# Kernel optimization log

Measured on AMD Instinct MI355X. Metric: run time of the kernel, lower is better.

Reference implementation:

```python
import jax, jax.numpy as jnp
import numpy as np

D_MODEL = 1024
N_LAYER = 8
VOCAB = 32000
D_INNER = 2048
D_STATE = 16
DT_RANK = 64  # ceil(d_model/16)
KCONV = 4
SEQ = 2048


def causal_depthwise_conv(u, w):
    # u: [l, d_inner], w: [d_inner, 1, K]; causal padding (K-1, 0), groups=d_inner
    x = u.T[None]  # [1, d_inner, l]
    y = jax.lax.conv_general_dilated(
        x, w, window_strides=(1,), padding=[(KCONV - 1, 0)],
        dimension_numbers=("NCH", "OIH", "NCH"), feature_group_count=u.shape[1])
    return y[0].T  # [l, d_inner]


def selective_scan(u, dt, A, B, C, Dp):
    # u,dt: [l,d_in]; A: [d_in,n]; B,C: [l,n]; D: [d_in]; bilinear discretization
    dt_A = dt[:, :, None] * A[None, :, :]          # [l, d_in, n]
    dt_B = dt[:, :, None] * B[:, None, :]          # [l, d_in, n]
    denom = 1.0 - dt_A / 2
    dA = (1.0 + dt_A / 2) / denom
    dB = dt_B / denom

    def step(h, inp):
        ui, dAi, dBi, Ci = inp
        h = dAi * h + dBi * ui[:, None]            # [d_in, n]
        return h, h @ Ci                           # y_i: [d_in]

    h0 = jnp.zeros((u.shape[1], A.shape[1]), dtype=u.dtype)
    _, y = jax.lax.scan(step, h0, (u, dA, dB, C))
    return y + u * Dp


def mamba_layer(x, Wres, Win, Wconv, WB, WC, Wdt1, Wdt2, bdt, logA, Dp, Wout):
    # RMS pre-norm (no learned scale)
    xn = x * jax.lax.rsqrt(jnp.mean(x * x, axis=-1, keepdims=True) + 1e-6)
    res = xn @ Wres.T                              # [l, d_inner]
    u = xn @ Win.T                                 # [l, d_inner]
    u = causal_depthwise_conv(u, Wconv)
    u = jax.nn.silu(u)
    A = -jnp.exp(logA)                             # [d_inner, n]
    B = u @ WB.T                                   # [l, n]
    C = u @ WC.T                                   # [l, n]
    dt = jax.nn.softplus((u @ Wdt1.T) @ Wdt2.T + bdt)
    y = selective_scan(u, dt, A, B, C, Dp)
    y = y * jax.nn.silu(res)
    return x + y @ Wout.T                          # residual


def setup_inputs() -> dict:
    key = jax.random.key(0)
    ks = jax.random.split(key, 12)
    L = N_LAYER
    token_ids = jax.random.randint(ks[0], (SEQ,), 0, VOCAB)
    embed = jax.random.normal(ks[1], (VOCAB, D_MODEL), jnp.float32) * 0.02
    Wres = jax.random.normal(ks[2], (L, D_INNER, D_MODEL), jnp.float32) * 0.02
    Win = jax.random.normal(ks[3], (L, D_INNER, D_MODEL), jnp.float32) * 0.02
    Wconv = jax.random.normal(ks[4], (L, D_INNER, 1, KCONV), jnp.float32) * 0.3
    WB = jax.random.normal(ks[5], (L, D_STATE, D_INNER), jnp.float32) * 0.02
    WC = jax.random.normal(ks[6], (L, D_STATE, D_INNER), jnp.float32) * 0.02
    Wdt1 = jax.random.normal(ks[7], (L, DT_RANK, D_INNER), jnp.float32) / np.sqrt(D_INNER)
    Wdt2 = jax.random.uniform(ks[8], (L, D_INNER, DT_RANK), jnp.float32,
                              minval=-1 / np.sqrt(DT_RANK), maxval=1 / np.sqrt(DT_RANK))
    # inverse-softplus of dt ~ U[1e-3, 1e-1] in log space
    dt0 = jnp.exp(jax.random.uniform(ks[9], (L, D_INNER)) * (np.log(0.1) - np.log(0.001)) + np.log(0.001))
    bdt = dt0 + jnp.log(-jnp.expm1(-dt0))
    logA = jnp.log(jnp.broadcast_to(jnp.arange(1, D_STATE + 1, dtype=jnp.float32),
                                    (L, D_INNER, D_STATE)))
    Dp = jnp.ones((L, D_INNER), jnp.float32)
    Wout = jax.random.normal(ks[10], (L, D_MODEL, D_INNER), jnp.float32) * 0.02
    return dict(token_ids=token_ids, embed=embed, Wres=Wres, Win=Win, Wconv=Wconv,
                WB=WB, WC=WC, Wdt1=Wdt1, Wdt2=Wdt2, bdt=bdt, logA=logA, Dp=Dp, Wout=Wout)


def reference(token_ids, embed, Wres, Win, Wconv, WB, WC, Wdt1, Wdt2, bdt, logA, Dp, Wout):
    x = embed[token_ids]  # [l, d_model]
    for i in range(Wres.shape[0]):
        x = mamba_layer(x, Wres[i], Win[i], Wconv[i], WB[i], WC[i],
                        Wdt1[i], Wdt2[i], bdt[i], logA[i], Dp[i], Wout[i])
    return x @ embed.T  # [l, vocab] logits (tied embedding)
```

## Files before the change

### kernel.cpp

```cpp
#include <hip/hip_runtime.h>

#define SEQ 2048
#define DMODEL 1024
#define DINNER 2048
#define DSTATE 16
#define DTRANK 64
#define NLAYER 8
#define VOCAB 32000
#define NCHUNK 32
#define CLEN 64
#define PZ 16

typedef float f32x4 __attribute__((ext_vector_type(4)));
typedef short bf16x8 __attribute__((ext_vector_type(8)));

__device__ __forceinline__ ushort f2bf(float f) {
  union { float f; unsigned u; } v; v.f = f;
  unsigned r = v.u + 0x7fffu + ((v.u >> 16) & 1u);
  return (ushort)(r >> 16);
}
__device__ __forceinline__ float bf2f(ushort b) {
  union { unsigned u; float f; } v; v.u = ((unsigned)b) << 16;
  return v.f;
}

__device__ __forceinline__ void lds_load16(const void* g, void* l) {
  __builtin_amdgcn_global_load_lds(
      (const __attribute__((address_space(1))) void*)g,
      (__attribute__((address_space(3))) void*)l, 16, 0, 0);
}

template<int BM, bool NTS>
__global__ __launch_bounds__(512, 2) void gemm8p_bt_bf16(
    const ushort* __restrict__ A, const ushort* __restrict__ B,
    float* __restrict__ C, int N, int K)
{
  constexpr int MFR = BM / 32;
  constexpr int MPP = MFR / 4;
  constexpr int ALOADS = BM / 128;
  __shared__ __align__(16) ushort As[2 * BM * 64];
  __shared__ __align__(16) ushort Bs[2 * 256 * 64];
  const int tid = threadIdx.x;
  const int lane = tid & 63;
  const int wid = tid >> 6;
  const int wr = wid >> 2, wc = wid & 3;
  const int rr = lane & 15, kq = lane >> 4;

  unsigned nwg = gridDim.x * gridDim.y;
  unsigned lb = blockIdx.y * gridDim.x + blockIdx.x;
  if ((nwg & 7u) == 0u) { unsigned cpx = nwg >> 3; lb = (lb & 7u) * cpx + (lb >> 3); }
  const int bm = (int)(lb % gridDim.x) * BM;
  const int bn = (int)(lb / gridDim.x) * 256;

  const ushort* Abase = A + (size_t)bm * K;
  const ushort* Bbase = B + (size_t)bn * K;

  auto stageA = [&](int buf, int h, int kt) {
    constexpr int HR = BM / 2;
#pragma unroll
    for (int L = 0; L < ALOADS; ++L) {
      int f = L * 512 + tid;
      int rl = f >> 3, g = f & 7;
      int gg = g ^ (rl & 7);
      lds_load16(Abase + (size_t)(h * HR + rl) * K + kt * 64 + gg * 8,
                 (void*)(As + buf * (BM * 64) + (h * HR + rl) * 64 + g * 8));
    }
  };
  auto stageB = [&](int buf, int h, int kt) {
#pragma unroll
    for (int L = 0; L < 2; ++L) {
      int f = L * 512 + tid;
      int rl = f >> 3, g = f & 7;
      int gg = g ^ (rl & 7);
      lds_load16(Bbase + (size_t)(h * 128 + rl) * K + kt * 64 + gg * 8,
                 (void*)(Bs + buf * (256 * 64) + (h * 128 + rl) * 64 + g * 8));
    }
  };
  auto rdA = [&](int buf, int r, int kbyte) {
    int sw = kbyte ^ ((r & 7) << 4);
    return *(const bf16x8*)(As + buf * (BM * 64) + r * 64 + (sw >> 1));
  };
  auto rdB = [&](int buf, int r, int kbyte) {
    int sw = kbyte ^ ((r & 7) << 4);
    return *(const bf16x8*)(Bs + buf * (256 * 64) + r * 64 + (sw >> 1));
  };

  f32x4 acc[MFR][4];
#pragma unroll
  for (int m = 0; m < MFR; ++m)
#pragma unroll
    for (int n = 0; n < 4; ++n) acc[m][n] = (f32x4){0.f, 0.f, 0.f, 0.f};

  const int NT = K >> 6;
  stageA(0, 0, 0); stageA(0, 1, 0); stageB(0, 0, 0); stageB(0, 1, 0);

  for (int t = 0; t < NT; ++t) {
    const int cur = t & 1;
    const bool more = (t + 1 < NT);
    if (more) stageA(cur ^ 1, 0, t + 1);
    if (more) {
      if constexpr (BM == 256) asm volatile("s_waitcnt vmcnt(2)" ::: "memory");
      else                     asm volatile("s_waitcnt vmcnt(1)" ::: "memory");
    } else {
      asm volatile("s_waitcnt vmcnt(0)" ::: "memory");
    }
    __syncthreads();

    bf16x8 bfr[4][2];
#pragma unroll
    for (int n = 0; n < 4; ++n)
#pragma unroll
      for (int kk = 0; kk < 2; ++kk)
        bfr[n][kk] = rdB(cur, wc * 64 + n * 16 + rr, kk * 64 + kq * 16);

#pragma unroll
    for (int mq = 0; mq < 4; ++mq) {
      if (mq == 1 && more) stageA(cur ^ 1, 1, t + 1);
      if (mq == 2 && more) stageB(cur ^ 1, 0, t + 1);
      if (mq == 3 && more) stageB(cur ^ 1, 1, t + 1);
      bf16x8 af[MPP][2];
#pragma unroll
      for (int mf = 0; mf < MPP; ++mf)
#pragma unroll
        for (int kk = 0; kk < 2; ++kk)
          af[mf][kk] = rdA(cur, wr * (BM / 2) + (mq * MPP + mf) * 16 + rr, kk * 64 + kq * 16);
      __builtin_amdgcn_s_setprio(1);
#pragma unroll
      for (int kk = 0; kk < 2; ++kk)
#pragma unroll
        for (int mf = 0; mf < MPP; ++mf)
#pragma unroll
          for (int n = 0; n < 4; ++n)
            acc[mq * MPP + mf][n] = __builtin_amdgcn_mfma_f32_16x16x32_bf16(
                af[mf][kk], bfr[n][kk], acc[mq * MPP + mf][n], 0, 0, 0);
      __builtin_amdgcn_s_setprio(0);
    }
    __syncthreads();
  }

  float* ep = (float*)Bs + wid * (16 * 68);
  const int cg = bn + wc * 64;
#pragma unroll
  for (int m = 0; m < MFR; ++m) {
    const int r0g = bm + wr * (BM / 2) + m * 16;
#pragma unroll
    for (int n = 0; n < 4; ++n)
#pragma unroll
      for (int j = 0; j < 4; ++j)
        ep[(kq * 4 + j) * 68 + n * 16 + rr] = acc[m][n][j];
#pragma unroll
    for (int i = 0; i < 4; ++i) {
      int row = i * 4 + kq;
      f32x4 v = *(const f32x4*)&ep[row * 68 + rr * 4];
      f32x4* dst = (f32x4*)&C[(size_t)(r0g + row) * N + cg + rr * 4];
      if constexpr (NTS) __builtin_nontemporal_store(v, dst);
      else *dst = v;
    }
  }
}

template<bool OUTBF>
__global__ __launch_bounds__(256, 2) void gemm2p_bt_bf16(
    const ushort* __restrict__ A, const ushort* __restrict__ B,
    void* __restrict__ Cv, int N, int K)
{
  __shared__ __align__(16) ushort As[2 * 128 * 64];
  __shared__ __align__(16) ushort Bs[2 * 128 * 64];
  const int tid = threadIdx.x;
  const int lane = tid & 63;
  const int wave = tid >> 6;
  const int wr = wave >> 1, wc = wave & 1;
  const int rr = lane & 15, kq = lane >> 4;

  unsigned nwg = gridDim.x * gridDim.y;
  unsigned lb = blockIdx.y * gridDim.x + blockIdx.x;
  if ((nwg & 7u) == 0u) { unsigned cpx = nwg >> 3; lb = (lb & 7u) * cpx + (lb >> 3); }
  const int bm = (int)(lb % gridDim.x) * 128;
  const int bn = (int)(lb / gridDim.x) * 128;

  const ushort* Abase = A + (size_t)bm * K;
  const ushort* Bbase = B + (size_t)bn * K;

  auto stage = [&](int buf, int kt) {
#pragma unroll
    for (int i = 0; i < 4; ++i) {
      int f = i * 256 + tid;
      int rl = f >> 3, g = f & 7;
      int gg = g ^ (rl & 7);
      lds_load16(Abase + (size_t)rl * K + kt * 64 + gg * 8,
                 (void*)(As + buf * 8192 + rl * 64 + g * 8));
      lds_load16(Bbase + (size_t)rl * K + kt * 64 + gg * 8,
                 (void*)(Bs + buf * 8192 + rl * 64 + g * 8));
    }
  };
  auto rdA = [&](int buf, int r, int kbyte) {
    int sw = kbyte ^ ((r & 7) << 4);
    return *(const bf16x8*)(As + buf * 8192 + r * 64 + (sw >> 1));
  };
  auto rdB = [&](int buf, int r, int kbyte) {
    int sw = kbyte ^ ((r & 7) << 4);
    return *(const bf16x8*)(Bs + buf * 8192 + r * 64 + (sw >> 1));
  };

  f32x4 acc[4][4];
#pragma unroll
  for (int m = 0; m < 4; ++m)
#pragma unroll
    for (int n = 0; n < 4; ++n) acc[m][n] = (f32x4){0.f, 0.f, 0.f, 0.f};

  const int NT = K >> 6;
  stage(0, 0);

  for (int t = 0; t < NT; ++t) {
    const int cur = t & 1;
    if (t + 1 < NT) {
      stage(cur ^ 1, t + 1);
      asm volatile("s_waitcnt vmcnt(8)" ::: "memory");
    } else {
      asm volatile("s_waitcnt vmcnt(0)" ::: "memory");
    }
    __syncthreads();
#pragma unroll
    for (int ks = 0; ks < 2; ++ks) {
      const int kbyte = ks * 64 + kq * 16;
      bf16x8 af[4], bfr[4];
#pragma unroll
      for (int m = 0; m < 4; ++m)
        af[m] = rdA(cur, wr * 64 + m * 16 + rr, kbyte);
#pragma unroll
      for (int n = 0; n < 4; ++n)
        bfr[n] = rdB(cur, wc * 64 + n * 16 + rr, kbyte);
      __builtin_amdgcn_s_setprio(1);
#pragma unroll
      for (int m = 0; m < 4; ++m)
#pragma unroll
        for (int n = 0; n < 4; ++n)
          acc[m][n] = __builtin_amdgcn_mfma_f32_16x16x32_bf16(af[m], bfr[n], acc[m][n], 0, 0, 0);
      __builtin_amdgcn_s_setprio(0);
    }
    __syncthreads();
  }

  float* ep = (float*)Bs + wave * (16 * 68);
  const int cg = bn + wc * 64;
#pragma unroll
  for (int m = 0; m < 4; ++m) {
    const int r0g = bm + wr * 64 + m * 16;
#pragma unroll
    for (int n = 0; n < 4; ++n)
#pragma unroll
      for (int j = 0; j < 4; ++j)
        ep[(kq * 4 + j) * 68 + n * 16 + rr] = acc[m][n][j];
#pragma unroll
    for (int i = 0; i < 4; ++i) {
      int row = i * 4 + kq;
      f32x4 v = *(const f32x4*)&ep[row * 68 + rr * 4];
      if constexpr (OUTBF) {
        ushort* C = (ushort*)Cv;
        ushort4 o = {f2bf(v.x), f2bf(v.y), f2bf(v.z), f2bf(v.w)};
        *(ushort4*)&C[(size_t)(r0g + row) * N + cg + rr * 4] = o;
      } else {
        float* C = (float*)Cv;
        *(f32x4*)&C[(size_t)(r0g + row) * N + cg + rr * 4] = v;
      }
    }
  }
}

__global__ __launch_bounds__(256) void gemm_btk_bf16(
    const ushort* __restrict__ A, const ushort* __restrict__ B,
    float* __restrict__ Cp, int M, int N, int K)
{
  __shared__ __align__(16) ushort As[128 * 64];
  __shared__ __align__(16) ushort Bs[128 * 64];
  const int tid = threadIdx.x;
  const int lane = tid & 63;
  const int wave = tid >> 6;
  const int wr = wave >> 1, wc = wave & 1;
  const int KC = K / gridDim.z;
  const int k0 = blockIdx.z * KC;

  unsigned nwg = gridDim.x * gridDim.y;
  unsigned lb = blockIdx.y * gridDim.x + blockIdx.x;
  if ((nwg & 7u) == 0u) {
    unsigned cpx = nwg >> 3;
    lb = (lb & 7u) * cpx + (lb >> 3);
  }
  const int bm = (lb % gridDim.x) * 128;
  const int bn = (lb / gridDim.x) * 128;
  const int rr = lane & 15, kq = lane >> 4;

  f32x4 acc[4][4];
#pragma unroll
  for (int m = 0; m < 4; ++m)
#pragma unroll
    for (int n = 0; n < 4; ++n) acc[m][n] = (f32x4){0.f, 0.f, 0.f, 0.f};

  for (int kt = 0; kt < KC; kt += 64) {
#pragma unroll
    for (int i = 0; i < 4; ++i) {
      int fb = i * 256 + tid;
      int row = fb >> 3, cb = fb & 7;
      lds_load16(A + (size_t)(bm + row) * K + k0 + kt + cb * 8, (void*)(As + (size_t)fb * 8));
      lds_load16(B + (size_t)(bn + row) * K + k0 + kt + cb * 8, (void*)(Bs + (size_t)fb * 8));
    }
    __syncthreads();
#pragma unroll
    for (int ks = 0; ks < 2; ++ks) {
      bf16x8 af[4], bfr[4];
      const int koff = ks * 32 + kq * 8;
#pragma unroll
      for (int m = 0; m < 4; ++m)
        af[m] = *(const bf16x8*)&As[(wr * 64 + m * 16 + rr) * 64 + koff];
#pragma unroll
      for (int n = 0; n < 4; ++n)
        bfr[n] = *(const bf16x8*)&Bs[(wc * 64 + n * 16 + rr) * 64 + koff];
#pragma unroll
      for (int m = 0; m < 4; ++m)
#pragma unroll
        for (int n = 0; n < 4; ++n)
          acc[m][n] = __builtin_amdgcn_mfma_f32_16x16x32_bf16(af[m], bfr[n], acc[m][n], 0, 0, 0);
    }
    __syncthreads();
  }
  float* C = Cp + (size_t)blockIdx.z * M * N;
#pragma unroll
  for (int m = 0; m < 4; ++m) {
    const int r0 = bm + wr * 64 + m * 16 + kq * 4;
#pragma unroll
    for (int n = 0; n < 4; ++n) {
      const int cc = bn + wc * 64 + n * 16 + rr;
#pragma unroll
      for (int j = 0; j < 4; ++j)
        C[(size_t)(r0 + j) * N + cc] = acc[m][n][j];
    }
  }
}

__global__ __launch_bounds__(256) void gemm_dt_bf16(
    const ushort* __restrict__ A, const ushort* __restrict__ W,
    const float* __restrict__ bias, ushort* __restrict__ dt)
{
  __shared__ __align__(16) ushort As[128 * 64];
  __shared__ __align__(16) ushort Bs[128 * 64];
  __shared__ float eps[4 * 16 * 68];
  const int tid = threadIdx.x;
  const int lane = tid & 63;
  const int wave = tid >> 6;
  const int wr = wave >> 1, wc = wave & 1;
  const int rr = lane & 15, kq = lane >> 4;
  const int bm = blockIdx.x * 128;
  const int bn = blockIdx.y * 128;

#pragma unroll
  for (int i = 0; i < 4; ++i) {
    int f = i * 256 + tid;
    int rl = f >> 3, g = f & 7;
    lds_load16(A + (size_t)(bm + rl) * DTRANK + g * 8, (void*)(As + (size_t)f * 8));
    lds_load16(W + (size_t)(bn + rl) * DTRANK + g * 8, (void*)(Bs + (size_t)f * 8));
  }
  asm volatile("s_waitcnt vmcnt(0)" ::: "memory");
  __syncthreads();

  f32x4 acc[4][4];
#pragma unroll
  for (int m = 0; m < 4; ++m)
#pragma unroll
    for (int n = 0; n < 4; ++n) acc[m][n] = (f32x4){0.f, 0.f, 0.f, 0.f};

#pragma unroll
  for (int ks = 0; ks < 2; ++ks) {
    bf16x8 af[4], bfr[4];
    const int koff = ks * 32 + kq * 8;
#pragma unroll
    for (int m = 0; m < 4; ++m)
      af[m] = *(const bf16x8*)&As[(wr * 64 + m * 16 + rr) * 64 + koff];
#pragma unroll
    for (int n = 0; n < 4; ++n)
      bfr[n] = *(const bf16x8*)&Bs[(wc * 64 + n * 16 + rr) * 64 + koff];
#pragma unroll
    for (int m = 0; m < 4; ++m)
#pragma unroll
      for (int n = 0; n < 4; ++n)
        acc[m][n] = __builtin_amdgcn_mfma_f32_16x16x32_bf16(af[m], bfr[n], acc[m][n], 0, 0, 0);
  }
  __syncthreads();

  float* ep = eps + wave * (16 * 68);
  const int cgb = bn + wc * 64 + rr * 4;
  float4 b4 = *(const float4*)&bias[cgb];
#pragma unroll
  for (int m = 0; m < 4; ++m) {
    const int r0g = bm + wr * 64 + m * 16;
#pragma unroll
    for (int n = 0; n < 4; ++n)
#pragma unroll
      for (int j = 0; j < 4; ++j)
        ep[(kq * 4 + j) * 68 + n * 16 + rr] = acc[m][n][j];
#pragma unroll
    for (int i = 0; i < 4; ++i) {
      int row = i * 4 + kq;
      f32x4 v = *(const f32x4*)&ep[row * 68 + rr * 4];
      float v0 = v.x + b4.x, v1 = v.y + b4.y, v2 = v.z + b4.z, v3 = v.w + b4.w;
      v0 = (v0 > 20.f) ? v0 : log1pf(expf(v0));
      v1 = (v1 > 20.f) ? v1 : log1pf(expf(v1));
      v2 = (v2 > 20.f) ? v2 : log1pf(expf(v2));
      v3 = (v3 > 20.f) ? v3 : log1pf(expf(v3));
      ushort4 o = {f2bf(v0), f2bf(v1), f2bf(v2), f2bf(v3)};
      *(ushort4*)&dt[(size_t)(r0g + row) * DINNER + cgb] = o;
    }
  }
}

__global__ __launch_bounds__(256) void add3_rms_kernel(
    const float* __restrict__ P0, const float* __restrict__ P1,
    float* __restrict__ x, ushort* __restrict__ dst, int donorm)
{
  size_t o = (size_t)blockIdx.x * (DMODEL / 4) + threadIdx.x;
  float4 a = ((const float4*)P0)[o];
  float4 b = ((const float4*)P1)[o];
  float4 c = ((float4*)x)[o];
  c.x += a.x + b.x; c.y += a.y + b.y; c.z += a.z + b.z; c.w += a.w + b.w;
  ((float4*)x)[o] = c;
  float sc = 1.f;
  if (donorm) {
    float s = c.x * c.x + c.y * c.y + c.z * c.z + c.w * c.w;
#pragma unroll
    for (int off = 32; off > 0; off >>= 1) s += __shfl_down(s, off);
    __shared__ float ws[4];
    if ((threadIdx.x & 63) == 0) ws[threadIdx.x >> 6] = s;
    __syncthreads();
    float tot = ws[0] + ws[1] + ws[2] + ws[3];
    sc = rsqrtf(tot * (1.0f / DMODEL) + 1e-6f);
  }
  ushort4 o4 = {f2bf(c.x * sc), f2bf(c.y * sc), f2bf(c.z * sc), f2bf(c.w * sc)};
  ((ushort4*)dst)[o] = o4;
}

__global__ __launch_bounds__(256) void gather_rms_kernel(
    const int* __restrict__ ids, const float* __restrict__ embed,
    float* __restrict__ x, ushort* __restrict__ xnb)
{
  int row = blockIdx.x;
  int id = ids[row];
  float4 v = ((const float4*)(embed + (size_t)id * DMODEL))[threadIdx.x];
  size_t o = (size_t)row * (DMODEL / 4) + threadIdx.x;
  ((float4*)x)[o] = v;
  float s = v.x * v.x + v.y * v.y + v.z * v.z + v.w * v.w;
#pragma unroll
  for (int off = 32; off > 0; off >>= 1) s += __shfl_down(s, off);
  __shared__ float ws[4];
  if ((threadIdx.x & 63) == 0) ws[threadIdx.x >> 6] = s;
  __syncthreads();
  float tot = ws[0] + ws[1] + ws[2] + ws[3];
  float sc = rsqrtf(tot * (1.0f / DMODEL) + 1e-6f);
  ushort4 o4 = {f2bf(v.x * sc), f2bf(v.y * sc), f2bf(v.z * sc), f2bf(v.w * sc)};
  ((ushort4*)xnb)[o] = o4;
}

__global__ __launch_bounds__(256) void proj_reduce(
    const float* __restrict__ Cp, float* __restrict__ bcdt,
    ushort* __restrict__ dtinb, int M)
{
  int idx = blockIdx.x * 256 + threadIdx.x;
  int row = idx / 96, col = idx - row * 96;
  float s = 0.f;
#pragma unroll
  for (int c = 0; c < PZ; ++c) s += Cp[(size_t)c * M * 128 + (size_t)row * 128 + col];
  if (col < 32) bcdt[(size_t)row * 96 + col] = s;
  else dtinb[(size_t)row * 64 + (col - 32)] = f2bf(s);
}

__global__ __launch_bounds__(256) void conv_silu_kernel(
    const ushort* __restrict__ u0, int ld, const float* __restrict__ Wconv,
    ushort* __restrict__ u)
{
  int idx = blockIdx.x * 256 + threadIdx.x;
  int d4 = idx & (DINNER / 4 - 1);
  int l = idx >> 9;
  int d0 = d4 * 4;
  float wt[4][4];
#pragma unroll
  for (int j = 0; j < 4; ++j) {
    float4 tv = *(const float4*)&Wconv[(d0 + j) * 4];
    wt[j][0] = tv.x; wt[j][1] = tv.y; wt[j][2] = tv.z; wt[j][3] = tv.w;
  }
  float a[4] = {0.f, 0.f, 0.f, 0.f};
#pragma unroll
  for (int k = 0; k < 4; ++k) {
    int ls = l - 3 + k;
    if (ls >= 0) {
      ushort4 uv = *(const ushort4*)&u0[(size_t)ls * ld + d0];
      a[0] += bf2f(uv.x) * wt[0][k];
      a[1] += bf2f(uv.y) * wt[1][k];
      a[2] += bf2f(uv.z) * wt[2][k];
      a[3] += bf2f(uv.w) * wt[3][k];
    }
  }
  float s0 = a[0] / (1.f + expf(-a[0]));
  float s1 = a[1] / (1.f + expf(-a[1]));
  float s2 = a[2] / (1.f + expf(-a[2]));
  float s3 = a[3] / (1.f + expf(-a[3]));
  ushort4 o = {f2bf(s0), f2bf(s1), f2bf(s2), f2bf(s3)};
  *(ushort4*)&u[(size_t)l * DINNER + d0] = o;
}

__global__ __launch_bounds__(256) void scan_pass1(
    const ushort* __restrict__ dt, const ushort* __restrict__ u,
    const float* __restrict__ bcdt, const float* __restrict__ logA,
    float* __restrict__ P, float* __restrict__ S)
{
  const int tid = threadIdx.x;
  const int n = tid & 15, dl = tid >> 4;
  const int dbase = blockIdx.x * 16;
  const int c = blockIdx.y;
  const int t0 = c * CLEN;
  const int d = dbase + dl;
  const float Aval = -expf(logA[d * DSTATE + n]);
  __shared__ float sdt[CLEN][16], su[CLEN][16], sB[CLEN][16];
  {
    int tt = tid >> 2, j0 = (tid & 3) * 4;
    ushort4 rd = *(const ushort4*)&dt[(size_t)(t0 + tt) * DINNER + dbase + j0];
    ushort4 ru = *(const ushort4*)&u[(size_t)(t0 + tt) * DINNER + dbase + j0];
    sdt[tt][j0 + 0] = bf2f(rd.x); sdt[tt][j0 + 1] = bf2f(rd.y);
    sdt[tt][j0 + 2] = bf2f(rd.z); sdt[tt][j0 + 3] = bf2f(rd.w);
    su[tt][j0 + 0] = bf2f(ru.x); su[tt][j0 + 1] = bf2f(ru.y);
    su[tt][j0 + 2] = bf2f(ru.z); su[tt][j0 + 3] = bf2f(ru.w);
    *(float4*)&sB[tt][j0] = *(const float4*)&bcdt[(size_t)(t0 + tt) * 96 + j0];
  }
  __syncthreads();
  float h = 0.f, pr = 1.f;
#pragma unroll 8
  for (int i = 0; i < CLEN; ++i) {
    float dtv = sdt[i][dl], uv = su[i][dl], Bv = sB[i][n];
    float dtA = dtv * Aval;
    float rinv = __builtin_amdgcn_rcpf(1.f - 0.5f * dtA);
    float dA = (1.f + 0.5f * dtA) * rinv;
    float dBu = dtv * Bv * rinv * uv;
    h = dA * h + dBu;
    pr *= dA;
  }
  size_t idx = (size_t)c * (DINNER * DSTATE) + (size_t)d * DSTATE + n;
  P[idx] = pr;
  S[idx] = h;
}

__global__ __launch_bounds__(256) void scan_pass2(
    const ushort* __restrict__ dt, const ushort* __restrict__ u,
    const float* __restrict__ bcdt, const float* __restrict__ logA,
    const float* __restrict__ Dp, const float* __restrict__ P,
    const float* __restrict__ S, const ushort* __restrict__ resu0,
    ushort* __restrict__ y2b)
{
  const int tid = threadIdx.x;
  const int n = tid & 15, dl = tid >> 4;
  const int dbase = blockIdx.x * 16;
  const int c = blockIdx.y;
  const int t0 = c * CLEN;
  const int d = dbase + dl;
  const float Aval = -expf(logA[d * DSTATE + n]);
  const float Dpv = Dp[d];
  __shared__ float sdt[CLEN][16], su[CLEN][16], sB[CLEN][16], sC[CLEN][16], sres[CLEN][16];
  {
    int tt = tid >> 2, j0 = (tid & 3) * 4;
    ushort4 rd = *(const ushort4*)&dt[(size_t)(t0 + tt) * DINNER + dbase + j0];
    ushort4 ru = *(const ushort4*)&u[(size_t)(t0 + tt) * DINNER + dbase + j0];
    ushort4 rr4 = *(const ushort4*)&resu0[(size_t)(t0 + tt) * (2 * DINNER) + dbase + j0];
    sdt[tt][j0 + 0] = bf2f(rd.x); sdt[tt][j0 + 1] = bf2f(rd.y);
    sdt[tt][j0 + 2] = bf2f(rd.z); sdt[tt][j0 + 3] = bf2f(rd.w);
    su[tt][j0 + 0] = bf2f(ru.x); su[tt][j0 + 1] = bf2f(ru.y);
    su[tt][j0 + 2] = bf2f(ru.z); su[tt][j0 + 3] = bf2f(ru.w);
    sres[tt][j0 + 0] = bf2f(rr4.x); sres[tt][j0 + 1] = bf2f(rr4.y);
    sres[tt][j0 + 2] = bf2f(rr4.z); sres[tt][j0 + 3] = bf2f(rr4.w);
    *(float4*)&sB[tt][j0] = *(const float4*)&bcdt[(size_t)(t0 + tt) * 96 + j0];
    *(float4*)&sC[tt][j0] = *(const float4*)&bcdt[(size_t)(t0 + tt) * 96 + 16 + j0];
  }
  float h = 0.f;
  {
    const size_t base = (size_t)d * DSTATE + n;
#pragma unroll 4
    for (int cc = 0; cc < c; ++cc) {
      size_t o = (size_t)cc * (DINNER * DSTATE) + base;
      h = P[o] * h + S[o];
    }
  }
  __syncthreads();
#pragma unroll 4
  for (int i = 0; i < CLEN; ++i) {
    float dtv = sdt[i][dl], uv = su[i][dl];
    float dtA = dtv * Aval;
    float rinv = __builtin_amdgcn_rcpf(1.f - 0.5f * dtA);
    float dA = (1.f + 0.5f * dtA) * rinv;
    float dBu = dtv * sB[i][n] * rinv * uv;
    h = dA * h + dBu;
    float p = h * sC[i][n];
    p += __shfl_xor(p, 1);
    p += __shfl_xor(p, 2);
    p += __shfl_xor(p, 4);
    p += __shfl_xor(p, 8);
    if (n == 0) {
      float rv = sres[i][dl];
      float yv = (p + uv * Dpv) * (rv / (1.f + expf(-rv)));
      y2b[(size_t)(t0 + i) * DINNER + d] = f2bf(yv);
    }
  }
}

__global__ __launch_bounds__(256) void cast_bf16_kernel(
    const float* __restrict__ in, ushort* __restrict__ out, size_t n4)
{
  size_t i = (size_t)blockIdx.x * 256 + threadIdx.x;
  if (i >= n4) return;
  float4 v = ((const float4*)in)[i];
  ushort4 o = {f2bf(v.x), f2bf(v.y), f2bf(v.z), f2bf(v.w)};
  ((ushort4*)out)[i] = o;
}

__global__ __launch_bounds__(256) void cast_cat2_kernel(
    const float* __restrict__ Wres, const float* __restrict__ Win, ushort* __restrict__ out)
{
  size_t i4 = (size_t)blockIdx.x * 256 + threadIdx.x;
  size_t e0 = i4 * 4;
  int k = (int)(e0 & (DMODEL - 1));
  int r = (int)((e0 >> 10) & (2 * DINNER - 1));
  int l = (int)(e0 >> 22);
  const float* src = (r < DINNER)
      ? &Wres[(((size_t)l * DINNER + r) << 10) + k]
      : &Win[(((size_t)l * DINNER + (r - DINNER)) << 10) + k];
  float4 v = *(const float4*)src;
  ushort4 o = {f2bf(v.x), f2bf(v.y), f2bf(v.z), f2bf(v.w)};
  ((ushort4*)out)[i4] = o;
}

__global__ __launch_bounds__(256) void concat_wbcdt_bf16_kernel(
    const float* __restrict__ WB, const float* __restrict__ WC,
    const float* __restrict__ Wdt1, ushort* __restrict__ out)
{
  size_t i4 = (size_t)blockIdx.x * 256 + threadIdx.x;
  int k4 = (int)(i4 & (DINNER / 4 - 1));
  int row = (int)((i4 >> 9) & 127);
  int l = (int)(i4 >> 16);
  int k = k4 * 4;
  float4 v = {0.f, 0.f, 0.f, 0.f};
  if (row < 16)       v = *(const float4*)&WB[((size_t)l * DSTATE + row) * DINNER + k];
  else if (row < 32)  v = *(const float4*)&WC[((size_t)l * DSTATE + (row - 16)) * DINNER + k];
  else if (row < 96)  v = *(const float4*)&Wdt1[((size_t)l * DTRANK + (row - 32)) * DINNER + k];
  ushort4 o = {f2bf(v.x), f2bf(v.y), f2bf(v.z), f2bf(v.w)};
  ((ushort4*)out)[i4] = o;
}

extern "C" void kernel_launch(void* const* d_in, const int* in_sizes, int n_in,
                              void* d_out, int out_size, void* d_ws, size_t ws_size,
                              hipStream_t stream) {
  (void)in_sizes; (void)n_in; (void)out_size;
  const int* token_ids = (const int*)d_in[0];
  const float* embed = (const float*)d_in[1];
  const float* Wres = (const float*)d_in[2];
  const float* Win = (const float*)d_in[3];
  const float* Wconv = (const float*)d_in[4];
  const float* WB = (const float*)d_in[5];
  const float* WC = (const float*)d_in[6];
  const float* Wdt1 = (const float*)d_in[7];
  const float* Wdt2 = (const float*)d_in[8];
  const float* bdt = (const float*)d_in[9];
  const float* logA = (const float*)d_in[10];
  const float* Dp = (const float*)d_in[11];
  const float* Wout = (const float*)d_in[12];
  float* out = (float*)d_out;

  char* w = (char*)d_ws;
  auto alloc = [&](size_t bytes) {
    char* p = w;
    w += (bytes + 255) & ~(size_t)255;
    return p;
  };
  ushort* eb     = (ushort*)alloc((size_t)VOCAB * DMODEL * 2);
  ushort* wcatb  = (ushort*)alloc((size_t)NLAYER * 2 * DINNER * DMODEL * 2);
  ushort* woutb  = (ushort*)alloc((size_t)NLAYER * DMODEL * DINNER * 2);
  ushort* wbcdtb = (ushort*)alloc((size_t)NLAYER * 128 * DINNER * 2);
  ushort* wdt2b  = (ushort*)alloc((size_t)NLAYER * DINNER * DTRANK * 2);
  float* x       = (float*)alloc((size_t)SEQ * DMODEL * 4);
  ushort* xnb    = (ushort*)alloc((size_t)SEQ * DMODEL * 2);
  ushort* resu0  = (ushort*)alloc((size_t)SEQ * 2 * DINNER * 2);
  ushort* u      = (ushort*)alloc((size_t)SEQ * DINNER * 2);
  float* bcdt    = (float*)alloc((size_t)SEQ * 96 * 4);
  ushort* dtinb  = (ushort*)alloc((size_t)SEQ * 64 * 2);
  ushort* dt     = (ushort*)alloc((size_t)SEQ * DINNER * 2);
  float* Cp      = (float*)alloc((size_t)PZ * SEQ * 128 * 4);
  float* Cp2     = (float*)alloc((size_t)2 * SEQ * DMODEL * 4);
  float* Pbuf    = (float*)alloc((size_t)NCHUNK * DINNER * DSTATE * 4);
  float* Sbuf    = (float*)alloc((size_t)NCHUNK * DINNER * DSTATE * 4);
  ushort* y2b    = (ushort*)alloc((size_t)SEQ * DINNER * 2);
  ushort* xb     = (ushort*)alloc((size_t)SEQ * DMODEL * 2);
  if ((size_t)(w - (char*)d_ws) > ws_size) return;

  cast_bf16_kernel<<<VOCAB * DMODEL / 4 / 256, 256, 0, stream>>>(embed, eb, (size_t)VOCAB * DMODEL / 4);
  cast_cat2_kernel<<<NLAYER * 2 * DINNER * DMODEL / 4 / 256, 256, 0, stream>>>(Wres, Win, wcatb);
  cast_bf16_kernel<<<NLAYER * DMODEL * DINNER / 4 / 256, 256, 0, stream>>>(Wout, woutb, (size_t)NLAYER * DMODEL * DINNER / 4);
  concat_wbcdt_bf16_kernel<<<NLAYER * 128 * DINNER / 4 / 256, 256, 0, stream>>>(WB, WC, Wdt1, wbcdtb);
  cast_bf16_kernel<<<NLAYER * DINNER * DTRANK / 4 / 256, 256, 0, stream>>>(Wdt2, wdt2b, (size_t)NLAYER * DINNER * DTRANK / 4);
  gather_rms_kernel<<<SEQ, 256, 0, stream>>>(token_ids, embed, x, xnb);

  for (int i = 0; i < NLAYER; ++i) {
    const ushort* wcati = wcatb + (size_t)i * 2 * DINNER * DMODEL;
    const ushort* wouti = woutb + (size_t)i * DMODEL * DINNER;
    const float* wconvi = Wconv + (size_t)i * DINNER * 4;
    const ushort* wbcdtbi = wbcdtb + (size_t)i * 128 * DINNER;
    const ushort* wdt2bi = wdt2b + (size_t)i * DINNER * DTRANK;
    const float* bdti = bdt + (size_t)i * DINNER;
    const float* logAi = logA + (size_t)i * DINNER * DSTATE;
    const float* Dpi = Dp + (size_t)i * DINNER;

    gemm2p_bt_bf16<true><<<dim3(SEQ / 128, 2 * DINNER / 128), 256, 0, stream>>>(
        xnb, wcati, resu0, 2 * DINNER, DMODEL);
    conv_silu_kernel<<<SEQ * DINNER / 4 / 256, 256, 0, stream>>>(resu0 + DINNER, 2 * DINNER, wconvi, u);
    gemm_btk_bf16<<<dim3(SEQ / 128, 1, PZ), 256, 0, stream>>>(
        u, wbcdtbi, Cp, SEQ, 128, DINNER);
    proj_reduce<<<SEQ * 96 / 256, 256, 0, stream>>>(Cp, bcdt, dtinb, SEQ);
    gemm_dt_bf16<<<dim3(SEQ / 128, DINNER / 128), 256, 0, stream>>>(
        dtinb, wdt2bi, bdti, dt);
    dim3 gs(DINNER / 16, NCHUNK);
    scan_pass1<<<gs, 256, 0, stream>>>(dt, u, bcdt, logAi, Pbuf, Sbuf);
    scan_pass2<<<gs, 256, 0, stream>>>(dt, u, bcdt, logAi, Dpi, Pbuf, Sbuf, resu0, y2b);
    gemm_btk_bf16<<<dim3(SEQ / 128, DMODEL / 128, 2), 256, 0, stream>>>(
        y2b, wouti, Cp2, SEQ, DMODEL, DINNER);
    add3_rms_kernel<<<SEQ, 256, 0, stream>>>(
        Cp2, Cp2 + (size_t)SEQ * DMODEL, x,
        (i < NLAYER - 1) ? xnb : xb, (i < NLAYER - 1) ? 1 : 0);
  }
  gemm8p_bt_bf16<256, true><<<dim3(SEQ / 256, VOCAB / 256), 512, 0, stream>>>(
      xb, eb, out, VOCAB, DMODEL);
}
```

Measured before the change: 1.996 ms.

## Fuse causal conv+SiLU into the B/C/dt projection GEMM and merge weight casts

```diff
diff --git a/kernel.cpp b/kernel.cpp
--- a/kernel.cpp
+++ b/kernel.cpp
@@ -337,6 +337,114 @@
   }
 }
 
+__global__ __launch_bounds__(256) void convproj_mfma(
+    const ushort* __restrict__ resu0, const ushort* __restrict__ W,
+    const float* __restrict__ Wconv, ushort* __restrict__ u,
+    float* __restrict__ Cp, int M)
+{
+  __shared__ __align__(16) ushort u0s[131][128];
+  __shared__ __align__(16) ushort As[2][128 * 64];
+  __shared__ __align__(16) ushort Bs[2][128 * 64];
+  const int tid = threadIdx.x;
+  const int lane = tid & 63;
+  const int wave = tid >> 6;
+  const int wr = wave >> 1, wc = wave & 1;
+  const int rr = lane & 15, kq = lane >> 4;
+  const int bm = blockIdx.x * 128;
+  const int kc = blockIdx.z * 128;
+
+#pragma unroll
+  for (int h = 0; h < 2; ++h)
+#pragma unroll
+    for (int i = 0; i < 4; ++i) {
+      int f = i * 256 + tid;
+      int rl = f >> 3, g = f & 7;
+      lds_load16(W + (size_t)rl * DINNER + kc + h * 64 + g * 8,
+                 (void*)(&Bs[h][rl * 64 + g * 8]));
+    }
+
+  for (int i = tid; i < 131 * 32; i += 256) {
+    int row = i >> 5, c4 = (i & 31) * 4;
+    int gr = bm - 3 + row;
+    ushort4 v = {0, 0, 0, 0};
+    if (gr >= 0)
+      v = *(const ushort4*)&resu0[(size_t)gr * (2 * DINNER) + DINNER + kc + c4];
+    *(ushort4*)&u0s[row][c4] = v;
+  }
+  __syncthreads();
+
+  {
+    const int c0 = (tid & 31) * 4;
+    const int r0 = (tid >> 5) * 16;
+    float4 w0 = *(const float4*)&Wconv[(kc + c0 + 0) * 4];
+    float4 w1 = *(const float4*)&Wconv[(kc + c0 + 1) * 4];
+    float4 w2 = *(const float4*)&Wconv[(kc + c0 + 2) * 4];
+    float4 w3 = *(const float4*)&Wconv[(kc + c0 + 3) * 4];
+    const int ks = c0 >> 6;
+    const int cl = c0 & 63;
+    for (int r = r0; r < r0 + 16; ++r) {
+      ushort4 a0 = *(const ushort4*)&u0s[r + 0][c0];
+      ushort4 a1 = *(const ushort4*)&u0s[r + 1][c0];
+      ushort4 a2 = *(const ushort4*)&u0s[r + 2][c0];
+      ushort4 a3 = *(const ushort4*)&u0s[r + 3][c0];
+      float o0 = bf2f(a0.x) * w0.x + bf2f(a1.x) * w0.y + bf2f(a2.x) * w0.z + bf2f(a3.x) * w0.w;
+      float o1 = bf2f(a0.y) * w1.x + bf2f(a1.y) * w1.y + bf2f(a2.y) * w1.z + bf2f(a3.y) * w1.w;
+      float o2 = bf2f(a0.z) * w2.x + bf2f(a1.z) * w2.y + bf2f(a2.z) * w2.z + bf2f(a3.z) * w2.w;
+      float o3 = bf2f(a0.w) * w3.x + bf2f(a1.w) * w3.y + bf2f(a2.w) * w3.z + bf2f(a3.w) * w3.w;
+      o0 = o0 / (1.f + expf(-o0));
+      o1 = o1 / (1.f + expf(-o1));
+      o2 = o2 / (1.f + expf(-o2));
+      o3 = o3 / (1.f + expf(-o3));
+      ushort4 o = {f2bf(o0), f2bf(o1), f2bf(o2), f2bf(o3)};
+      *(ushort4*)&As[ks][r * 64 + cl] = o;
+      *(ushort4*)&u[(size_t)(bm + r) * DINNER + kc + c0] = o;
+    }
+  }
+  asm volatile("s_waitcnt vmcnt(0)" ::: "memory");
+  __syncthreads();
+
+  f32x4 acc[4][4];
+#pragma unroll
+  for (int m = 0; m < 4; ++m)
+#pragma unroll
+    for (int n = 0; n < 4; ++n) acc[m][n] = (f32x4){0.f, 0.f, 0.f, 0.f};
+
+#pragma unroll
+  for (int ks = 0; ks < 2; ++ks) {
+#pragma unroll
+    for (int kk = 0; kk < 2; ++kk) {
+      const int koff = kk * 32 + kq * 8;
+      bf16x8 af[4], bfr[4];
+#pragma unroll
+      for (int m = 0; m < 4; ++m)
+        af[m] = *(const bf16x8*)&As[ks][(wr * 64 + m * 16 + rr) * 64 + koff];
+#pragma unroll
+      for (int n = 0; n < 4; ++n)
+        bfr[n] = *(const bf16x8*)&Bs[ks][(wc * 64 + n * 16 + rr) * 64 + koff];
+      __builtin_amdgcn_s_setprio(1);
+#pragma unroll
+      for (int m = 0; m < 4; ++m)
+#pragma unroll
+        for (int n = 0; n < 4; ++n)
+          acc[m][n] = __builtin_amdgcn_mfma_f32_16x16x32_bf16(af[m], bfr[n], acc[m][n], 0, 0, 0);
+      __builtin_amdgcn_s_setprio(0);
+    }
+  }
+
+  float* C = Cp + (size_t)blockIdx.z * M * 128;
+#pragma unroll
+  for (int m = 0; m < 4; ++m) {
+    const int r0 = bm + wr * 64 + m * 16 + kq * 4;
+#pragma unroll
+    for (int n = 0; n < 4; ++n) {
+      const int cc = wc * 64 + n * 16 + rr;
+#pragma unroll
+      for (int j = 0; j < 4; ++j)
+        C[(size_t)(r0 + j) * 128 + cc] = acc[m][n][j];
+    }
+  }
+}
+
 __global__ __launch_bounds__(256) void gemm_dt_bf16(
     const ushort* __restrict__ A, const ushort* __restrict__ W,
     const float* __restrict__ bias, ushort* __restrict__ dt)
@@ -469,40 +577,6 @@
   for (int c = 0; c < PZ; ++c) s += Cp[(size_t)c * M * 128 + (size_t)row * 128 + col];
   if (col < 32) bcdt[(size_t)row * 96 + col] = s;
   else dtinb[(size_t)row * 64 + (col - 32)] = f2bf(s);
-}
-
-__global__ __launch_bounds__(256) void conv_silu_kernel(
-    const ushort* __restrict__ u0, int ld, const float* __restrict__ Wconv,
-    ushort* __restrict__ u)
-{
-  int idx = blockIdx.x * 256 + threadIdx.x;
-  int d4 = idx & (DINNER / 4 - 1);
-  int l = idx >> 9;
-  int d0 = d4 * 4;
-  float wt[4][4];
-#pragma unroll
-  for (int j = 0; j < 4; ++j) {
-    float4 tv = *(const float4*)&Wconv[(d0 + j) * 4];
-    wt[j][0] = tv.x; wt[j][1] = tv.y; wt[j][2] = tv.z; wt[j][3] = tv.w;
-  }
-  float a[4] = {0.f, 0.f, 0.f, 0.f};
-#pragma unroll
-  for (int k = 0; k < 4; ++k) {
-    int ls = l - 3 + k;
-    if (ls >= 0) {
-      ushort4 uv = *(const ushort4*)&u0[(size_t)ls * ld + d0];
-      a[0] += bf2f(uv.x) * wt[0][k];
-      a[1] += bf2f(uv.y) * wt[1][k];
-      a[2] += bf2f(uv.z) * wt[2][k];
-      a[3] += bf2f(uv.w) * wt[3][k];
-    }
-  }
-  float s0 = a[0] / (1.f + expf(-a[0]));
-  float s1 = a[1] / (1.f + expf(-a[1]));
-  float s2 = a[2] / (1.f + expf(-a[2]));
-  float s3 = a[3] / (1.f + expf(-a[3]));
-  ushort4 o = {f2bf(s0), f2bf(s1), f2bf(s2), f2bf(s3)};
-  *(ushort4*)&u[(size_t)l * DINNER + d0] = o;
 }
 
 __global__ __launch_bounds__(256) void scan_pass1(
@@ -606,47 +680,62 @@
   }
 }
 
-__global__ __launch_bounds__(256) void cast_bf16_kernel(
-    const float* __restrict__ in, ushort* __restrict__ out, size_t n4)
-{
-  size_t i = (size_t)blockIdx.x * 256 + threadIdx.x;
-  if (i >= n4) return;
-  float4 v = ((const float4*)in)[i];
+__global__ __launch_bounds__(256) void preproc_kernel(
+    const float* __restrict__ embed, const float* __restrict__ Wres,
+    const float* __restrict__ Win, const float* __restrict__ Wout,
+    const float* __restrict__ WB, const float* __restrict__ WC,
+    const float* __restrict__ Wdt1, const float* __restrict__ Wdt2,
+    ushort* __restrict__ eb, ushort* __restrict__ wcatb,
+    ushort* __restrict__ woutb, ushort* __restrict__ wbcdtb,
+    ushort* __restrict__ wdt2b)
+{
+  const size_t S0 = (size_t)VOCAB * DMODEL / 4;
+  const size_t S1 = (size_t)NLAYER * 2 * DINNER * DMODEL / 4;
+  const size_t S2 = (size_t)NLAYER * DMODEL * DINNER / 4;
+  const size_t S3 = (size_t)NLAYER * 128 * DINNER / 4;
+  const size_t S4 = (size_t)NLAYER * DINNER * DTRANK / 4;
+  size_t i4 = (size_t)blockIdx.x * 256 + threadIdx.x;
+  float4 v;
+  ushort* dst;
+  size_t di;
+  if (i4 < S0) {
+    v = ((const float4*)embed)[i4];
+    dst = eb; di = i4;
+  } else if (i4 < S0 + S1) {
+    size_t j4 = i4 - S0;
+    size_t e0 = j4 * 4;
+    int k = (int)(e0 & (DMODEL - 1));
+    int r = (int)((e0 >> 10) & (2 * DINNER - 1));
+    int l = (int)(e0 >> 22);
+    const float* src = (r < DINNER)
+        ? &Wres[(((size_t)l * DINNER + r) << 10) + k]
+        : &Win[(((size_t)l * DINNER + (r - DINNER)) << 10) + k];
+    v = *(const float4*)src;
+    dst = wcatb; di = j4;
+  } else if (i4 < S0 + S1 + S2) {
+    size_t j4 = i4 - S0 - S1;
+    v = ((const float4*)Wout)[j4];
+    dst = woutb; di = j4;
+  } else if (i4 < S0 + S1 + S2 + S3) {
+    size_t j4 = i4 - S0 - S1 - S2;
+    int k4 = (int)(j4 & (DINNER / 4 - 1));
+    int row = (int)((j4 >> 9) & 127);
+    int l = (int)(j4 >> 16);
+    int k = k4 * 4;
+    v = (float4){0.f, 0.f, 0.f, 0.f};
+    if (row < 16)       v = *(const float4*)&WB[((size_t)l * DSTATE + row) * DINNER + k];
+    else if (row < 32)  v = *(const float4*)&WC[((size_t)l * DSTATE + (row - 16)) * DINNER + k];
+    else if (row < 96)  v = *(const float4*)&Wdt1[((size_t)l * DTRANK + (row - 32)) * DINNER + k];
+    dst = wbcdtb; di = j4;
+  } else if (i4 < S0 + S1 + S2 + S3 + S4) {
+    size_t j4 = i4 - S0 - S1 - S2 - S3;
+    v = ((const float4*)Wdt2)[j4];
+    dst = wdt2b; di = j4;
+  } else {
+    return;
+  }
   ushort4 o = {f2bf(v.x), f2bf(v.y), f2bf(v.z), f2bf(v.w)};
-  ((ushort4*)out)[i] = o;
-}
-
-__global__ __launch_bounds__(256) void cast_cat2_kernel(
-    const float* __restrict__ Wres, const float* __restrict__ Win, ushort* __restrict__ out)
-{
-  size_t i4 = (size_t)blockIdx.x * 256 + threadIdx.x;
-  size_t e0 = i4 * 4;
-  int k = (int)(e0 & (DMODEL - 1));
-  int r = (int)((e0 >> 10) & (2 * DINNER - 1));
-  int l = (int)(e0 >> 22);
-  const float* src = (r < DINNER)
-      ? &Wres[(((size_t)l * DINNER + r) << 10) + k]
-      : &Win[(((size_t)l * DINNER + (r - DINNER)) << 10) + k];
-  float4 v = *(const float4*)src;
-  ushort4 o = {f2bf(v.x), f2bf(v.y), f2bf(v.z), f2bf(v.w)};
-  ((ushort4*)out)[i4] = o;
-}
-
-__global__ __launch_bounds__(256) void concat_wbcdt_bf16_kernel(
-    const float* __restrict__ WB, const float* __restrict__ WC,
-    const float* __restrict__ Wdt1, ushort* __restrict__ out)
-{
-  size_t i4 = (size_t)blockIdx.x * 256 + threadIdx.x;
-  int k4 = (int)(i4 & (DINNER / 4 - 1));
-  int row = (int)((i4 >> 9) & 127);
-  int l = (int)(i4 >> 16);
-  int k = k4 * 4;
-  float4 v = {0.f, 0.f, 0.f, 0.f};
-  if (row < 16)       v = *(const float4*)&WB[((size_t)l * DSTATE + row) * DINNER + k];
-  else if (row < 32)  v = *(const float4*)&WC[((size_t)l * DSTATE + (row - 16)) * DINNER + k];
-  else if (row < 96)  v = *(const float4*)&Wdt1[((size_t)l * DTRANK + (row - 32)) * DINNER + k];
-  ushort4 o = {f2bf(v.x), f2bf(v.y), f2bf(v.z), f2bf(v.w)};
-  ((ushort4*)out)[i4] = o;
+  ((ushort4*)dst)[di] = o;
 }
 
 extern "C" void kernel_launch(void* const* d_in, const int* in_sizes, int n_in,
@@ -694,11 +783,17 @@
   ushort* xb     = (ushort*)alloc((size_t)SEQ * DMODEL * 2);
   if ((size_t)(w - (char*)d_ws) > ws_size) return;
 
-  cast_bf16_kernel<<<VOCAB * DMODEL / 4 / 256, 256, 0, stream>>>(embed, eb, (size_t)VOCAB * DMODEL / 4);
-  cast_cat2_kernel<<<NLAYER * 2 * DINNER * DMODEL / 4 / 256, 256, 0, stream>>>(Wres, Win, wcatb);
-  cast_bf16_kernel<<<NLAYER * DMODEL * DINNER / 4 / 256, 256, 0, stream>>>(Wout, woutb, (size_t)NLAYER * DMODEL * DINNER / 4);
-  concat_wbcdt_bf16_kernel<<<NLAYER * 128 * DINNER / 4 / 256, 256, 0, stream>>>(WB, WC, Wdt1, wbcdtb);
-  cast_bf16_kernel<<<NLAYER * DINNER * DTRANK / 4 / 256, 256, 0, stream>>>(Wdt2, wdt2b, (size_t)NLAYER * DINNER * DTRANK / 4);
+  {
+    size_t total4 = (size_t)VOCAB * DMODEL / 4
+                  + (size_t)NLAYER * 2 * DINNER * DMODEL / 4
+                  + (size_t)NLAYER * DMODEL * DINNER / 4
+                  + (size_t)NLAYER * 128 * DINNER / 4
+                  + (size_t)NLAYER * DINNER * DTRANK / 4;
+    int nblk = (int)((total4 + 255) / 256);
+    preproc_kernel<<<nblk, 256, 0, stream>>>(
+        embed, Wres, Win, Wout, WB, WC, Wdt1, Wdt2,
+        eb, wcatb, woutb, wbcdtb, wdt2b);
+  }
   gather_rms_kernel<<<SEQ, 256, 0, stream>>>(token_ids, embed, x, xnb);
 
   for (int i = 0; i < NLAYER; ++i) {
@@ -713,9 +808,8 @@
 
     gemm2p_bt_bf16<true><<<dim3(SEQ / 128, 2 * DINNER / 128), 256, 0, stream>>>(
         xnb, wcati, resu0, 2 * DINNER, DMODEL);
-    conv_silu_kernel<<<SEQ * DINNER / 4 / 256, 256, 0, stream>>>(resu0 + DINNER, 2 * DINNER, wconvi, u);
-    gemm_btk_bf16<<<dim3(SEQ / 128, 1, PZ), 256, 0, stream>>>(
-        u, wbcdtbi, Cp, SEQ, 128, DINNER);
+    convproj_mfma<<<dim3(SEQ / 128, 1, PZ), 256, 0, stream>>>(
+        resu0, wbcdtbi, wconvi, u, Cp, SEQ);
     proj_reduce<<<SEQ * 96 / 256, 256, 0, stream>>>(Cp, bcdt, dtinb, SEQ);
     gemm_dt_bf16<<<dim3(SEQ / 128, DINNER / 128), 256, 0, stream>>>(
         dtinb, wdt2bi, bdti, dt);
```

Result: faster. 1.940 ms (-2.8%).
